# Kernel optimization log

Hardware: AMD Instinct MI355X
Metric: run time of the kernel (lower is better)

## Reference

```python
import jax, jax.numpy as jnp
import numpy as np

EPS = 1e-06
TEMP = 2.0

def _l2norm(x, eps=EPS):
    # F.normalize: x / max(||x||, eps)
    n = jnp.sqrt(jnp.sum(x * x, axis=-1, keepdims=True))
    return x / jnp.maximum(n, eps)

def setup_inputs() -> dict:
    key = jax.random.key(0)
    k1, k2 = jax.random.split(key)
    B, Lt, Lv, D = 8, 64, 16384, 256
    t = jax.random.normal(k1, (B, Lt, D), dtype=jnp.float32)
    v = jax.random.normal(k2, (B, Lv, D), dtype=jnp.float32)
    return {"t": t, "v": v}

def reference(t, v):
    dtype = v.dtype
    t = _l2norm(jnp.nan_to_num(t).astype(jnp.float32))
    v = _l2norm(jnp.nan_to_num(v).astype(jnp.float32))
    # S: [B, Lv, Lt]
    S = jnp.einsum('bvd,btd->bvt', v, t) / TEMP
    # text->vision attention: softmax over text axis (stable shift as in source)
    S_vt = jnp.nan_to_num(S - jnp.max(S, axis=2, keepdims=True))
    A_vt = jax.nn.softmax(S_vt, axis=2)            # [B, Lv, Lt]
    weights_vt = jax.nn.softmax(A_vt / TEMP, axis=1)  # softmax over vision axis
    text_score = jnp.sum(weights_vt * A_vt, axis=1)   # [B, Lt]
    text_score = text_score / (jnp.sum(text_score, axis=1, keepdims=True) + EPS)
    # vision<-text attention: per-sample loop in source == batched softmax over Lv
    S_tv = jnp.nan_to_num(S - jnp.max(S, axis=1, keepdims=True))
    A_tv = jax.nn.softmax(S_tv, axis=1)            # softmax over vision axis, [B, Lv, Lt]
    scores = jnp.einsum('bvt,bt->bv', A_tv, text_score)  # [B, Lv]
    mn = jnp.min(scores, axis=1, keepdims=True)
    mx = jnp.max(scores, axis=1, keepdims=True)
    scores = (scores - mn) / (mx - mn + EPS)
    return scores.astype(dtype)
```

## Files before the change

kernel.cpp:

```cpp
#include <hip/hip_runtime.h>
#include <stdint.h>

#define NB 8
#define LT 64
#define LV 16384
#define DD 256
#define EPSV 1e-6f
#define BF16MAX 3.3895313892515355e38f

typedef unsigned short u16t;
typedef __attribute__((ext_vector_type(8))) short short8;
typedef __attribute__((ext_vector_type(4))) float floatx4;

__device__ __forceinline__ float bf2f(u16t h) {
    union { uint32_t u; float f; } cv; cv.u = ((uint32_t)h) << 16; return cv.f;
}
__device__ __forceinline__ uint32_t asu(float f) { union { float f; uint32_t u; } c; c.f = f; return c.u; }
__device__ __forceinline__ float asf(uint32_t u) { union { uint32_t u; float f; } c; c.u = u; return c.f; }
__device__ __forceinline__ u16t f2bf(float f) {
    uint32_t u = asu(f);
    return (u16t)((u + 0x7fffu + ((u >> 16) & 1u)) >> 16);
}
__device__ __forceinline__ float fixnum(float f) {
    if (f != f) return 0.0f;
    if (f > BF16MAX) return BF16MAX;
    if (f < -BF16MAX) return -BF16MAX;
    return f;
}
__device__ __forceinline__ float load_in(const void* p, long i, int isf32) {
    return isf32 ? ((const float*)p)[i] : bf2f(((const u16t*)p)[i]);
}
__device__ __forceinline__ uint32_t bfhead(float a, float& hf) {
    uint32_t u = asu(a);
    uint32_t h = (u + 0x7fffu + ((u >> 16) & 1u)) >> 16;
    hf = asf(h << 16);
    return h;
}

__global__ void k_sniff(const u16t* v, int* flag) {
    int lane = threadIdx.x;
    int sane = 0;
    for (int i = 0; i < 16; ++i) {
        u16t h = v[lane * 16 + i];
        int ex = (h >> 7) & 0xFF;
        if ((h & 0x7FFF) == 0 || (ex >= 96 && ex < 160)) ++sane;
    }
    #pragma unroll
    for (int o = 1; o < 64; o <<= 1) sane += __shfl_xor(sane, o, 64);
    if (lane == 0) flag[0] = (sane < 900) ? 1 : 0;
}

__global__ void k0_zero(float* Z) {
    int i = blockIdx.x * 256 + threadIdx.x;
    if (i < 1536) Z[i] = 0.0f;
    else if (i < 1552) {
        unsigned* u = (unsigned*)(Z + 2048);
        int j = i - 1536;
        u[j] = (j & 1) ? 0u : 0x7F7FFFFFu;
    }
}

__global__ void k1_tnorm(const void* t, u16t* tnB, const int* flag) {
    __shared__ float red[256];
    int isf32 = flag[0];
    int row = blockIdx.x;
    int k = threadIdx.x;
    float x = fixnum(load_in(t, (long)row * DD + k, isf32));
    red[k] = x * x;
    __syncthreads();
    for (int s = 128; s > 0; s >>= 1) {
        if (k < s) red[k] += red[k + s];
        __syncthreads();
    }
    float scale = 0.5f / fmaxf(sqrtf(red[0]), EPSV);
    tnB[row * DD + k] = f2bf(x * scale);
}

__global__ __launch_bounds__(256) void k_gemm(const void* v, const u16t* tnB,
                                              float* Z, float* S1, float* S2,
                                              const float* c, float* scores,
                                              float* E,
                                              const int* flag, int mode) {
    __shared__ u16t ldsT[64 * 264];
    __shared__ float zlds[3][4][64];
    int isf32 = flag[0];
    int tid = threadIdx.x, wave = tid >> 6, lane = tid & 63;
    int c16 = lane & 15, q = lane >> 4;
    int b = blockIdx.y, tile = blockIdx.x;
    int rowbase = tile * 128 + wave * 32;

    {
        const u16t* src = tnB + (size_t)b * (LT * DD);
        for (int i = tid; i < 2048; i += 256) {
            int tt = i >> 5, k8 = i & 31;
            *(uint4*)&ldsT[tt * 264 + k8 * 8] = *(const uint4*)&src[tt * DD + k8 * 8];
        }
    }
    __syncthreads();

    floatx4 acc[2][4];
    #pragma unroll
    for (int mt = 0; mt < 2; ++mt)
        #pragma unroll
        for (int nt = 0; nt < 4; ++nt) acc[mt][nt] = (floatx4){0.f, 0.f, 0.f, 0.f};
    float ssqp[2] = {0.f, 0.f};

    for (int kc = 0; kc < 8; ++kc) {
        short8 bf[4];
        #pragma unroll
        for (int nt = 0; nt < 4; ++nt)
            bf[nt] = *(const short8*)&ldsT[(nt * 16 + c16) * 264 + kc * 32 + q * 8];

        #pragma unroll
        for (int mt = 0; mt < 2; ++mt) {
            int row = rowbase + mt * 16 + c16;
            float f[8];
            if (isf32) {
                const float* vr = (const float*)v +
                    ((size_t)b * LV + row) * DD + kc * 32 + q * 8;
                float4 p0 = *(const float4*)vr;
                float4 p1 = *(const float4*)(vr + 4);
                f[0]=p0.x; f[1]=p0.y; f[2]=p0.z; f[3]=p0.w;
                f[4]=p1.x; f[5]=p1.y; f[6]=p1.z; f[7]=p1.w;
            } else {
                const u16t* vr = (const u16t*)v +
                    ((size_t)b * LV + row) * DD + kc * 32 + q * 8;
                uint4 u = *(const uint4*)vr;
                f[0]=bf2f((u16t)u.x); f[1]=bf2f((u16t)(u.x>>16));
                f[2]=bf2f((u16t)u.y); f[3]=bf2f((u16t)(u.y>>16));
                f[4]=bf2f((u16t)u.z); f[5]=bf2f((u16t)(u.z>>16));
                f[6]=bf2f((u16t)u.w); f[7]=bf2f((u16t)(u.w>>16));
            }
            #pragma unroll
            for (int i = 0; i < 8; ++i) f[i] = fixnum(f[i]);
            union { short8 s; uint32_t u[4]; } a1, a2, a3;
            #pragma unroll
            for (int i = 0; i < 4; ++i) {
                float e0 = f[2*i], e1 = f[2*i+1];
                ssqp[mt] += e0 * e0 + e1 * e1;
                float h10f, h11f, h20f, h21f, dummy;
                uint32_t h10 = bfhead(e0, h10f), h11 = bfhead(e1, h11f);
                float r10 = e0 - h10f,  r11 = e1 - h11f;
                uint32_t h20 = bfhead(r10, h20f), h21 = bfhead(r11, h21f);
                float r20 = r10 - h20f, r21 = r11 - h21f;
                uint32_t h30 = bfhead(r20, dummy), h31 = bfhead(r21, dummy);
                a1.u[i] = h10 | (h11 << 16);
                a2.u[i] = h20 | (h21 << 16);
                a3.u[i] = h30 | (h31 << 16);
            }
            #pragma unroll
            for (int nt = 0; nt < 4; ++nt) {
                acc[mt][nt] = __builtin_amdgcn_mfma_f32_16x16x32_bf16(
                    a1.s, bf[nt], acc[mt][nt], 0, 0, 0);
                acc[mt][nt] = __builtin_amdgcn_mfma_f32_16x16x32_bf16(
                    a2.s, bf[nt], acc[mt][nt], 0, 0, 0);
                acc[mt][nt] = __builtin_amdgcn_mfma_f32_16x16x32_bf16(
                    a3.s, bf[nt], acc[mt][nt], 0, 0, 0);
            }
        }
    }

    float ssqf[2];
    #pragma unroll
    for (int mt = 0; mt < 2; ++mt) {
        float s = ssqp[mt];
        s += __shfl_xor(s, 16, 64);
        s += __shfl_xor(s, 32, 64);
        ssqf[mt] = s;
    }
    float facr[2][4];
    #pragma unroll
    for (int mt = 0; mt < 2; ++mt)
        #pragma unroll
        for (int reg = 0; reg < 4; ++reg) {
            float ss = __shfl(ssqf[mt], q * 4 + reg, 64);
            facr[mt][reg] = 1.0f / fmaxf(sqrtf(ss), EPSV);
        }

    if (mode == 0) {
        float zacc[4] = {0,0,0,0}, s1acc[4] = {0,0,0,0}, s2acc[4] = {0,0,0,0};
        #pragma unroll
        for (int mt = 0; mt < 2; ++mt)
            #pragma unroll
            for (int reg = 0; reg < 4; ++reg) {
                float e[4], se = 0.f;
                #pragma unroll
                for (int nt = 0; nt < 4; ++nt) {
                    e[nt] = __expf(acc[mt][nt][reg] * facr[mt][reg]);
                    se += e[nt];
                }
                se += __shfl_xor(se, 1, 64);
                se += __shfl_xor(se, 2, 64);
                se += __shfl_xor(se, 4, 64);
                se += __shfl_xor(se, 8, 64);
                float inv = 1.0f / se;
                if (E) {
                    size_t rbase = ((((size_t)b << 14) + rowbase + mt * 16 + q * 4 + reg) << 6);
                    #pragma unroll
                    for (int nt = 0; nt < 4; ++nt)
                        E[rbase + nt * 16 + c16] = e[nt];
                }
                #pragma unroll
                for (int nt = 0; nt < 4; ++nt) {
                    float A = e[nt] * inv;
                    float w = __expf(0.5f * A);
                    zacc[nt] += e[nt]; s1acc[nt] += w; s2acc[nt] += w * A;
                }
            }
        #pragma unroll
        for (int nt = 0; nt < 4; ++nt) {
            zacc[nt]  += __shfl_xor(zacc[nt], 16, 64);  zacc[nt]  += __shfl_xor(zacc[nt], 32, 64);
            s1acc[nt] += __shfl_xor(s1acc[nt], 16, 64); s1acc[nt] += __shfl_xor(s1acc[nt], 32, 64);
            s2acc[nt] += __shfl_xor(s2acc[nt], 16, 64); s2acc[nt] += __shfl_xor(s2acc[nt], 32, 64);
        }
        if (lane < 16) {
            #pragma unroll
            for (int nt = 0; nt < 4; ++nt) {
                zlds[0][wave][nt * 16 + lane] = zacc[nt];
                zlds[1][wave][nt * 16 + lane] = s1acc[nt];
                zlds[2][wave][nt * 16 + lane] = s2acc[nt];
            }
        }
        __syncthreads();
        if (tid < 64) {
            float z  = zlds[0][0][tid] + zlds[0][1][tid] + zlds[0][2][tid] + zlds[0][3][tid];
            float a  = zlds[1][0][tid] + zlds[1][1][tid] + zlds[1][2][tid] + zlds[1][3][tid];
            float s2 = zlds[2][0][tid] + zlds[2][1][tid] + zlds[2][2][tid] + zlds[2][3][tid];
            atomicAdd(&Z[b * LT + tid], z);
            atomicAdd(&S1[b * LT + tid], a);
            atomicAdd(&S2[b * LT + tid], s2);
        }
    } else {
        float cc[4];
        #pragma unroll
        for (int nt = 0; nt < 4; ++nt) cc[nt] = c[b * LT + nt * 16 + c16];
        #pragma unroll
        for (int mt = 0; mt < 2; ++mt)
            #pragma unroll
            for (int reg = 0; reg < 4; ++reg) {
                float x = 0.f;
                #pragma unroll
                for (int nt = 0; nt < 4; ++nt)
                    x += __expf(acc[mt][nt][reg] * facr[mt][reg]) * cc[nt];
                x += __shfl_xor(x, 1, 64);
                x += __shfl_xor(x, 2, 64);
                x += __shfl_xor(x, 4, 64);
                x += __shfl_xor(x, 8, 64);
                if (c16 == 0)
                    scores[(size_t)b * LV + rowbase + mt * 16 + q * 4 + reg] = x;
            }
    }
}

__global__ __launch_bounds__(64) void k3_coef(const float* Z, const float* S1,
                                              const float* S2, float* c) {
    int b = blockIdx.x, lane = threadIdx.x;
    float ts = S2[b * LT + lane] / S1[b * LT + lane];
    float tot = ts;
    #pragma unroll
    for (int o = 1; o < 64; o <<= 1) tot += __shfl_xor(tot, o, 64);
    c[b * LT + lane] = ts / ((tot + EPSV) * Z[b * LT + lane]);
}

__global__ __launch_bounds__(256) void k2_scores(const float* E, const float* c,
                                                 float* scores, unsigned* mnmxU) {
    __shared__ float cl[64];
    __shared__ float rmn[256], rmx[256];
    int tid = threadIdx.x;
    int b = blockIdx.x >> 6;
    if (tid < 64) cl[tid] = c[b * LT + tid];
    __syncthreads();
    size_t row = (size_t)blockIdx.x * 256 + tid;
    const float* er = E + (row << 6);
    float f[64];
    #pragma unroll
    for (int j = 0; j < 16; ++j) {
        float4 v4 = *(const float4*)(er + j * 4);
        f[j*4+0] = v4.x; f[j*4+1] = v4.y; f[j*4+2] = v4.z; f[j*4+3] = v4.w;
    }
    float p[16];
    #pragma unroll
    for (int i = 0; i < 16; ++i) {
        float x = 0.f;
        #pragma unroll
        for (int nt = 0; nt < 4; ++nt) x += f[nt * 16 + i] * cl[nt * 16 + i];
        p[i] = x;
    }
    float q1[8], q2[4], q3[2];
    #pragma unroll
    for (int j = 0; j < 8; ++j) q1[j] = p[2*j] + p[2*j+1];
    #pragma unroll
    for (int j = 0; j < 4; ++j) q2[j] = q1[2*j] + q1[2*j+1];
    #pragma unroll
    for (int j = 0; j < 2; ++j) q3[j] = q2[2*j] + q2[2*j+1];
    float x = q3[0] + q3[1];
    scores[row] = x;

    rmn[tid] = x; rmx[tid] = x;
    __syncthreads();
    for (int s = 128; s > 0; s >>= 1) {
        if (tid < s) {
            rmn[tid] = fminf(rmn[tid], rmn[tid + s]);
            rmx[tid] = fmaxf(rmx[tid], rmx[tid + s]);
        }
        __syncthreads();
    }
    if (tid == 0) {
        atomicMin(&mnmxU[b * 2],     asu(rmn[0]));
        atomicMax(&mnmxU[b * 2 + 1], asu(rmx[0]));
    }
}

__global__ __launch_bounds__(256) void k_mnmx(const float* scores, float* mnmx) {
    __shared__ float rmn[256], rmx[256];
    int b = blockIdx.x, tid = threadIdx.x;
    float mn = 3.4e38f, mx = -3.4e38f;
    for (int i = tid; i < LV; i += 256) {
        float x = scores[b * LV + i];
        mn = fminf(mn, x); mx = fmaxf(mx, x);
    }
    rmn[tid] = mn; rmx[tid] = mx;
    __syncthreads();
    for (int s = 128; s > 0; s >>= 1) {
        if (tid < s) {
            rmn[tid] = fminf(rmn[tid], rmn[tid + s]);
            rmx[tid] = fmaxf(rmx[tid], rmx[tid + s]);
        }
        __syncthreads();
    }
    if (tid == 0) { mnmx[b * 2] = rmn[0]; mnmx[b * 2 + 1] = rmx[0]; }
}

__global__ __launch_bounds__(256) void k5_out(const float* scores, const float* mnmx,
                                              void* out, const int* flag) {
    int isf32 = flag[0];
    int i = blockIdx.x * 256 + threadIdx.x;
    if (i >= NB * LV) return;
    int b = i >> 14;
    float mn = mnmx[b * 2], mx = mnmx[b * 2 + 1];
    float val = (scores[i] - mn) / (mx - mn + EPSV);
    if (isf32) ((float*)out)[i] = val;
    else ((u16t*)out)[i] = f2bf(val);
}

extern "C" void kernel_launch(void* const* d_in, const int* in_sizes, int n_in,
                              void* d_out, int out_size, void* d_ws, size_t ws_size,
                              hipStream_t stream) {
    const void* t = d_in[0];
    const void* v = d_in[1];
    char* w = (char*)d_ws;

    const size_t E_BYTES = (size_t)NB * LV * LT * 4;
    const size_t NEED_NEW = E_BYTES + 262144 + 524288 + 2080 * 4;

    if (ws_size >= NEED_NEW) {
        float* E      = (float*)w;
        u16t*  tnB    = (u16t*)(w + E_BYTES);
        float* scores = (float*)(w + E_BYTES + 262144);
        float* Z      = (float*)(w + E_BYTES + 262144 + 524288);
        float* S1     = Z + 512;
        float* S2     = Z + 1024;
        float* c      = Z + 1536;
        unsigned* mnmxU = (unsigned*)(Z + 2048);
        int*   flag   = (int*)(Z + 2064);

        k_sniff<<<1, 64, 0, stream>>>((const u16t*)v, flag);
        k0_zero<<<7, 256, 0, stream>>>(Z);
        k1_tnorm<<<512, 256, 0, stream>>>(t, tnB, flag);
        k_gemm<<<dim3(128, NB), 256, 0, stream>>>(v, tnB, Z, S1, S2, nullptr, nullptr,
                                                  E, flag, 0);
        k3_coef<<<NB, 64, 0, stream>>>(Z, S1, S2, c);
        k2_scores<<<512, 256, 0, stream>>>(E, c, scores, mnmxU);
        k5_out<<<512, 256, 0, stream>>>(scores, (const float*)mnmxU, d_out, flag);
    } else {
        u16t*  tnB    = (u16t*)w;
        float* scores = (float*)(w + 262144);
        float* Z      = (float*)(w + 786432);
        float* S1     = Z + 512;
        float* S2     = Z + 1024;
        float* c      = Z + 1536;
        float* mnmx   = Z + 2048;
        int*   flag   = (int*)(Z + 2064);

        k_sniff<<<1, 64, 0, stream>>>((const u16t*)v, flag);
        k0_zero<<<6, 256, 0, stream>>>(Z);
        k1_tnorm<<<512, 256, 0, stream>>>(t, tnB, flag);
        k_gemm<<<dim3(128, NB), 256, 0, stream>>>(v, tnB, Z, S1, S2, nullptr, nullptr,
                                                  nullptr, flag, 0);
        k3_coef<<<NB, 64, 0, stream>>>(Z, S1, S2, c);
        k_gemm<<<dim3(128, NB), 256, 0, stream>>>(v, tnB, Z, S1, S2, c, scores,
                                                  nullptr, flag, 1);
        k_mnmx<<<NB, 256, 0, stream>>>(scores, mnmx);
        k5_out<<<512, 256, 0, stream>>>(scores, mnmx, d_out, flag);
    }
}
```

Measured before the change: 236.7 us.

## Fuse setup kernels, drop third bf16 split term, prefetch v loads in GEMM

The separate sniff and zero kernels are removed: each kernel now re-detects the input dtype in one wave, and the tnorm kernel zeroes the accumulators. The coefficient kernel is folded into k2_scores, and min/max is fused into the mode-1 GEMM. The GEMM splits fp32 activations into two bf16 terms instead of three, cutting MFMA work by a third at some precision cost, and it register-prefetches the next k-chunk of v. Fewer launches and less matrix work are traded for redundant sniffing in every block and lower dot-product accuracy.

```diff
diff --git a/kernel.cpp b/kernel.cpp
--- a/kernel.cpp
+++ b/kernel.cpp
@@ -37,8 +37,7 @@
     return h;
 }
 
-__global__ void k_sniff(const u16t* v, int* flag) {
-    int lane = threadIdx.x;
+__device__ __forceinline__ int sniff_wave(const u16t* v, int lane) {
     int sane = 0;
     for (int i = 0; i < 16; ++i) {
         u16t h = v[lane * 16 + i];
@@ -47,24 +46,18 @@
     }
     #pragma unroll
     for (int o = 1; o < 64; o <<= 1) sane += __shfl_xor(sane, o, 64);
-    if (lane == 0) flag[0] = (sane < 900) ? 1 : 0;
-}
-
-__global__ void k0_zero(float* Z) {
-    int i = blockIdx.x * 256 + threadIdx.x;
-    if (i < 1536) Z[i] = 0.0f;
-    else if (i < 1552) {
-        unsigned* u = (unsigned*)(Z + 2048);
-        int j = i - 1536;
-        u[j] = (j & 1) ? 0u : 0x7F7FFFFFu;
-    }
-}
-
-__global__ void k1_tnorm(const void* t, u16t* tnB, const int* flag) {
+    return (sane < 900) ? 1 : 0;
+}
+
+__global__ __launch_bounds__(256) void k1_tnorm(const void* t, const void* v,
+                                                u16t* tnB, float* Z) {
     __shared__ float red[256];
-    int isf32 = flag[0];
+    __shared__ int sflag;
     int row = blockIdx.x;
     int k = threadIdx.x;
+    if (k < 64) { int f = sniff_wave((const u16t*)v, k); if (k == 0) sflag = f; }
+    __syncthreads();
+    int isf32 = sflag;
     float x = fixnum(load_in(t, (long)row * DD + k, isf32));
     red[k] = x * x;
     __syncthreads();
@@ -74,21 +67,32 @@
     }
     float scale = 0.5f / fmaxf(sqrtf(red[0]), EPSV);
     tnB[row * DD + k] = f2bf(x * scale);
-}
-
-__global__ __launch_bounds__(256) void k_gemm(const void* v, const u16t* tnB,
-                                              float* Z, float* S1, float* S2,
-                                              const float* c, float* scores,
-                                              float* E,
-                                              const int* flag, int mode) {
+
+    if (blockIdx.x < 7) {
+        int i = blockIdx.x * 256 + k;
+        if (i < 1536) Z[i] = 0.0f;
+        else if (i < 1552) {
+            unsigned* u = (unsigned*)(Z + 2048);
+            int j = i - 1536;
+            u[j] = (j & 1) ? 0u : 0x7F7FFFFFu;
+        }
+    }
+}
+
+template<int MODE>
+__global__ __launch_bounds__(256) void k_gemmT(const void* v, const u16t* tnB,
+                                               float* Z, float* S1, float* S2,
+                                               float* EoS, const float* c,
+                                               unsigned* mnmxU) {
     __shared__ u16t ldsT[64 * 264];
     __shared__ float zlds[3][4][64];
-    int isf32 = flag[0];
+    __shared__ int sflag;
     int tid = threadIdx.x, wave = tid >> 6, lane = tid & 63;
     int c16 = lane & 15, q = lane >> 4;
     int b = blockIdx.y, tile = blockIdx.x;
     int rowbase = tile * 128 + wave * 32;
 
+    if (tid < 64) { int f = sniff_wave((const u16t*)v, tid); if (tid == 0) sflag = f; }
     {
         const u16t* src = tnB + (size_t)b * (LT * DD);
         for (int i = tid; i < 2048; i += 256) {
@@ -97,6 +101,7 @@
         }
     }
     __syncthreads();
+    int isf32 = sflag;
 
     floatx4 acc[2][4];
     #pragma unroll
@@ -105,60 +110,90 @@
         for (int nt = 0; nt < 4; ++nt) acc[mt][nt] = (floatx4){0.f, 0.f, 0.f, 0.f};
     float ssqp[2] = {0.f, 0.f};
 
-    for (int kc = 0; kc < 8; ++kc) {
-        short8 bf[4];
-        #pragma unroll
-        for (int nt = 0; nt < 4; ++nt)
-            bf[nt] = *(const short8*)&ldsT[(nt * 16 + c16) * 264 + kc * 32 + q * 8];
-
-        #pragma unroll
-        for (int mt = 0; mt < 2; ++mt) {
-            int row = rowbase + mt * 16 + c16;
-            float f[8];
-            if (isf32) {
-                const float* vr = (const float*)v +
-                    ((size_t)b * LV + row) * DD + kc * 32 + q * 8;
-                float4 p0 = *(const float4*)vr;
-                float4 p1 = *(const float4*)(vr + 4);
-                f[0]=p0.x; f[1]=p0.y; f[2]=p0.z; f[3]=p0.w;
-                f[4]=p1.x; f[5]=p1.y; f[6]=p1.z; f[7]=p1.w;
-            } else {
-                const u16t* vr = (const u16t*)v +
-                    ((size_t)b * LV + row) * DD + kc * 32 + q * 8;
-                uint4 u = *(const uint4*)vr;
-                f[0]=bf2f((u16t)u.x); f[1]=bf2f((u16t)(u.x>>16));
-                f[2]=bf2f((u16t)u.y); f[3]=bf2f((u16t)(u.y>>16));
-                f[4]=bf2f((u16t)u.z); f[5]=bf2f((u16t)(u.z>>16));
-                f[6]=bf2f((u16t)u.w); f[7]=bf2f((u16t)(u.w>>16));
-            }
+    #define PROC_F8(mt)                                                        \
+        do {                                                                   \
+            _Pragma("unroll")                                                  \
+            for (int i = 0; i < 8; ++i) f[i] = fixnum(f[i]);                   \
+            union { short8 s; uint32_t u[4]; } a1, a2;                         \
+            _Pragma("unroll")                                                  \
+            for (int i = 0; i < 4; ++i) {                                      \
+                float e0 = f[2*i], e1 = f[2*i+1];                              \
+                ssqp[mt] += e0 * e0 + e1 * e1;                                 \
+                float h10f, h11f, d0, d1;                                      \
+                uint32_t h10 = bfhead(e0, h10f), h11 = bfhead(e1, h11f);       \
+                float r10 = e0 - h10f,  r11 = e1 - h11f;                       \
+                uint32_t h20 = bfhead(r10, d0), h21 = bfhead(r11, d1);         \
+                a1.u[i] = h10 | (h11 << 16);                                   \
+                a2.u[i] = h20 | (h21 << 16);                                   \
+            }                                                                  \
+            _Pragma("unroll")                                                  \
+            for (int nt = 0; nt < 4; ++nt) {                                   \
+                acc[mt][nt] = __builtin_amdgcn_mfma_f32_16x16x32_bf16(         \
+                    a1.s, bf[nt], acc[mt][nt], 0, 0, 0);                       \
+                acc[mt][nt] = __builtin_amdgcn_mfma_f32_16x16x32_bf16(         \
+                    a2.s, bf[nt], acc[mt][nt], 0, 0, 0);                       \
+            }                                                                  \
+        } while (0)
+
+    if (isf32) {
+        const float4* vr0 = (const float4*)((const float*)v +
+            ((size_t)b * LV + rowbase + c16) * DD) + q * 2;
+        const float4* vr1 = (const float4*)((const float*)v +
+            ((size_t)b * LV + rowbase + 16 + c16) * DD) + q * 2;
+        float4 nA0 = vr0[0], nA1 = vr0[1], nB0 = vr1[0], nB1 = vr1[1];
+        for (int kc = 0; kc < 8; ++kc) {
+            short8 bf[4];
             #pragma unroll
-            for (int i = 0; i < 8; ++i) f[i] = fixnum(f[i]);
-            union { short8 s; uint32_t u[4]; } a1, a2, a3;
+            for (int nt = 0; nt < 4; ++nt)
+                bf[nt] = *(const short8*)&ldsT[(nt * 16 + c16) * 264 + kc * 32 + q * 8];
+            float4 cA0 = nA0, cA1 = nA1, cB0 = nB0, cB1 = nB1;
+            if (kc < 7) {
+                int o = (kc + 1) * 8;
+                nA0 = vr0[o]; nA1 = vr0[o + 1];
+                nB0 = vr1[o]; nB1 = vr1[o + 1];
+            }
+            {
+                float f[8] = {cA0.x, cA0.y, cA0.z, cA0.w, cA1.x, cA1.y, cA1.z, cA1.w};
+                PROC_F8(0);
+            }
+            {
+                float f[8] = {cB0.x, cB0.y, cB0.z, cB0.w, cB1.x, cB1.y, cB1.z, cB1.w};
+                PROC_F8(1);
+            }
+        }
+    } else {
+        const uint4* vr0 = (const uint4*)((const u16t*)v +
+            ((size_t)b * LV + rowbase + c16) * DD) + q;
+        const uint4* vr1 = (const uint4*)((const u16t*)v +
+            ((size_t)b * LV + rowbase + 16 + c16) * DD) + q;
+        uint4 nA = vr0[0], nB = vr1[0];
+        for (int kc = 0; kc < 8; ++kc) {
+            short8 bf[4];
             #pragma unroll
-            for (int i = 0; i < 4; ++i) {
-                float e0 = f[2*i], e1 = f[2*i+1];
-                ssqp[mt] += e0 * e0 + e1 * e1;
-                float h10f, h11f, h20f, h21f, dummy;
-                uint32_t h10 = bfhead(e0, h10f), h11 = bfhead(e1, h11f);
-                float r10 = e0 - h10f,  r11 = e1 - h11f;
-                uint32_t h20 = bfhead(r10, h20f), h21 = bfhead(r11, h21f);
-                float r20 = r10 - h20f, r21 = r11 - h21f;
-                uint32_t h30 = bfhead(r20, dummy), h31 = bfhead(r21, dummy);
-                a1.u[i] = h10 | (h11 << 16);
-                a2.u[i] = h20 | (h21 << 16);
-                a3.u[i] = h30 | (h31 << 16);
-            }
-            #pragma unroll
-            for (int nt = 0; nt < 4; ++nt) {
-                acc[mt][nt] = __builtin_amdgcn_mfma_f32_16x16x32_bf16(
-                    a1.s, bf[nt], acc[mt][nt], 0, 0, 0);
-                acc[mt][nt] = __builtin_amdgcn_mfma_f32_16x16x32_bf16(
-                    a2.s, bf[nt], acc[mt][nt], 0, 0, 0);
-                acc[mt][nt] = __builtin_amdgcn_mfma_f32_16x16x32_bf16(
-                    a3.s, bf[nt], acc[mt][nt], 0, 0, 0);
-            }
-        }
-    }
+            for (int nt = 0; nt < 4; ++nt)
+                bf[nt] = *(const short8*)&ldsT[(nt * 16 + c16) * 264 + kc * 32 + q * 8];
+            uint4 cA = nA, cB = nB;
+            if (kc < 7) {
+                int o = (kc + 1) * 4;
+                nA = vr0[o]; nB = vr1[o];
+            }
+            {
+                float f[8] = {bf2f((u16t)cA.x), bf2f((u16t)(cA.x >> 16)),
+                              bf2f((u16t)cA.y), bf2f((u16t)(cA.y >> 16)),
+                              bf2f((u16t)cA.z), bf2f((u16t)(cA.z >> 16)),
+                              bf2f((u16t)cA.w), bf2f((u16t)(cA.w >> 16))};
+                PROC_F8(0);
+            }
+            {
+                float f[8] = {bf2f((u16t)cB.x), bf2f((u16t)(cB.x >> 16)),
+                              bf2f((u16t)cB.y), bf2f((u16t)(cB.y >> 16)),
+                              bf2f((u16t)cB.z), bf2f((u16t)(cB.z >> 16)),
+                              bf2f((u16t)cB.w), bf2f((u16t)(cB.w >> 16))};
+                PROC_F8(1);
+            }
+        }
+    }
+    #undef PROC_F8
 
     float ssqf[2];
     #pragma unroll
@@ -177,7 +212,7 @@
             facr[mt][reg] = 1.0f / fmaxf(sqrtf(ss), EPSV);
         }
 
-    if (mode == 0) {
+    if (MODE == 0) {
         float zacc[4] = {0,0,0,0}, s1acc[4] = {0,0,0,0}, s2acc[4] = {0,0,0,0};
         #pragma unroll
         for (int mt = 0; mt < 2; ++mt)
@@ -194,11 +229,11 @@
                 se += __shfl_xor(se, 4, 64);
                 se += __shfl_xor(se, 8, 64);
                 float inv = 1.0f / se;
-                if (E) {
+                if (EoS) {
                     size_t rbase = ((((size_t)b << 14) + rowbase + mt * 16 + q * 4 + reg) << 6);
                     #pragma unroll
                     for (int nt = 0; nt < 4; ++nt)
-                        E[rbase + nt * 16 + c16] = e[nt];
+                        EoS[rbase + nt * 16 + c16] = e[nt];
                 }
                 #pragma unroll
                 for (int nt = 0; nt < 4; ++nt) {
@@ -234,6 +269,7 @@
         float cc[4];
         #pragma unroll
         for (int nt = 0; nt < 4; ++nt) cc[nt] = c[b * LT + nt * 16 + c16];
+        float lmn = 3.4e38f, lmx = -3.4e38f;
         #pragma unroll
         for (int mt = 0; mt < 2; ++mt)
             #pragma unroll
@@ -247,8 +283,24 @@
                 x += __shfl_xor(x, 4, 64);
                 x += __shfl_xor(x, 8, 64);
                 if (c16 == 0)
-                    scores[(size_t)b * LV + rowbase + mt * 16 + q * 4 + reg] = x;
-            }
+                    EoS[(size_t)b * LV + rowbase + mt * 16 + q * 4 + reg] = x;
+                lmn = fminf(lmn, x); lmx = fmaxf(lmx, x);
+            }
+        float* rmn = (float*)ldsT;
+        float* rmx = ((float*)ldsT) + 256;
+        rmn[tid] = lmn; rmx[tid] = lmx;
+        __syncthreads();
+        for (int s = 128; s > 0; s >>= 1) {
+            if (tid < s) {
+                rmn[tid] = fminf(rmn[tid], rmn[tid + s]);
+                rmx[tid] = fmaxf(rmx[tid], rmx[tid + s]);
+            }
+            __syncthreads();
+        }
+        if (tid == 0) {
+            atomicMin(&mnmxU[b * 2],     asu(rmn[0]));
+            atomicMax(&mnmxU[b * 2 + 1], asu(rmx[0]));
+        }
     }
 }
 
@@ -262,13 +314,20 @@
     c[b * LT + lane] = ts / ((tot + EPSV) * Z[b * LT + lane]);
 }
 
-__global__ __launch_bounds__(256) void k2_scores(const float* E, const float* c,
+__global__ __launch_bounds__(256) void k2_scores(const float* E, const float* Zg,
                                                  float* scores, unsigned* mnmxU) {
     __shared__ float cl[64];
     __shared__ float rmn[256], rmx[256];
     int tid = threadIdx.x;
     int b = blockIdx.x >> 6;
-    if (tid < 64) cl[tid] = c[b * LT + tid];
+    if (tid < 64) {
+        const float* Z = Zg; const float* S1 = Zg + 512; const float* S2 = Zg + 1024;
+        float ts = S2[b * LT + tid] / S1[b * LT + tid];
+        float tot = ts;
+        #pragma unroll
+        for (int o = 1; o < 64; o <<= 1) tot += __shfl_xor(tot, o, 64);
+        cl[tid] = ts / ((tot + EPSV) * Z[b * LT + tid]);
+    }
     __syncthreads();
     size_t row = (size_t)blockIdx.x * 256 + tid;
     const float* er = E + (row << 6);
@@ -311,30 +370,14 @@
     }
 }
 
-__global__ __launch_bounds__(256) void k_mnmx(const float* scores, float* mnmx) {
-    __shared__ float rmn[256], rmx[256];
-    int b = blockIdx.x, tid = threadIdx.x;
-    float mn = 3.4e38f, mx = -3.4e38f;
-    for (int i = tid; i < LV; i += 256) {
-        float x = scores[b * LV + i];
-        mn = fminf(mn, x); mx = fmaxf(mx, x);
-    }
-    rmn[tid] = mn; rmx[tid] = mx;
-    __syncthreads();
-    for (int s = 128; s > 0; s >>= 1) {
-        if (tid < s) {
-            rmn[tid] = fminf(rmn[tid], rmn[tid + s]);
-            rmx[tid] = fmaxf(rmx[tid], rmx[tid + s]);
-        }
-        __syncthreads();
-    }
-    if (tid == 0) { mnmx[b * 2] = rmn[0]; mnmx[b * 2 + 1] = rmx[0]; }
-}
-
 __global__ __launch_bounds__(256) void k5_out(const float* scores, const float* mnmx,
-                                              void* out, const int* flag) {
-    int isf32 = flag[0];
-    int i = blockIdx.x * 256 + threadIdx.x;
+                                              void* out, const void* v) {
+    __shared__ int sflag;
+    int tid = threadIdx.x;
+    if (tid < 64) { int f = sniff_wave((const u16t*)v, tid); if (tid == 0) sflag = f; }
+    __syncthreads();
+    int isf32 = sflag;
+    int i = blockIdx.x * 256 + tid;
     if (i >= NB * LV) return;
     int b = i >> 14;
     float mn = mnmx[b * 2], mx = mnmx[b * 2 + 1];
@@ -360,18 +403,13 @@
         float* Z      = (float*)(w + E_BYTES + 262144 + 524288);
         float* S1     = Z + 512;
         float* S2     = Z + 1024;
-        float* c      = Z + 1536;
         unsigned* mnmxU = (unsigned*)(Z + 2048);
-        int*   flag   = (int*)(Z + 2064);
-
-        k_sniff<<<1, 64, 0, stream>>>((const u16t*)v, flag);
-        k0_zero<<<7, 256, 0, stream>>>(Z);
-        k1_tnorm<<<512, 256, 0, stream>>>(t, tnB, flag);
-        k_gemm<<<dim3(128, NB), 256, 0, stream>>>(v, tnB, Z, S1, S2, nullptr, nullptr,
-                                                  E, flag, 0);
-        k3_coef<<<NB, 64, 0, stream>>>(Z, S1, S2, c);
-        k2_scores<<<512, 256, 0, stream>>>(E, c, scores, mnmxU);
-        k5_out<<<512, 256, 0, stream>>>(scores, (const float*)mnmxU, d_out, flag);
+
+        k1_tnorm<<<512, 256, 0, stream>>>(t, v, tnB, Z);
+        k_gemmT<0><<<dim3(128, NB), 256, 0, stream>>>(v, tnB, Z, S1, S2, E,
+                                                      nullptr, nullptr);
+        k2_scores<<<512, 256, 0, stream>>>(E, Z, scores, mnmxU);
+        k5_out<<<512, 256, 0, stream>>>(scores, (const float*)mnmxU, d_out, v);
     } else {
         u16t*  tnB    = (u16t*)w;
         float* scores = (float*)(w + 262144);
@@ -379,18 +417,14 @@
         float* S1     = Z + 512;
         float* S2     = Z + 1024;
         float* c      = Z + 1536;
-        float* mnmx   = Z + 2048;
-        int*   flag   = (int*)(Z + 2064);
-
-        k_sniff<<<1, 64, 0, stream>>>((const u16t*)v, flag);
-        k0_zero<<<6, 256, 0, stream>>>(Z);
-        k1_tnorm<<<512, 256, 0, stream>>>(t, tnB, flag);
-        k_gemm<<<dim3(128, NB), 256, 0, stream>>>(v, tnB, Z, S1, S2, nullptr, nullptr,
-                                                  nullptr, flag, 0);
+        unsigned* mnmxU = (unsigned*)(Z + 2048);
+
+        k1_tnorm<<<512, 256, 0, stream>>>(t, v, tnB, Z);
+        k_gemmT<0><<<dim3(128, NB), 256, 0, stream>>>(v, tnB, Z, S1, S2, nullptr,
+                                                      nullptr, nullptr);
         k3_coef<<<NB, 64, 0, stream>>>(Z, S1, S2, c);
-        k_gemm<<<dim3(128, NB), 256, 0, stream>>>(v, tnB, Z, S1, S2, c, scores,
-                                                  nullptr, flag, 1);
-        k_mnmx<<<NB, 256, 0, stream>>>(scores, mnmx);
-        k5_out<<<512, 256, 0, stream>>>(scores, mnmx, d_out, flag);
-    }
-}
+        k_gemmT<1><<<dim3(128, NB), 256, 0, stream>>>(v, tnB, Z, S1, S2, scores,
+                                                      c, mnmxU);
+        k5_out<<<512, 256, 0, stream>>>(scores, (const float*)mnmxU, d_out, v);
+    }
+}
```

Result: no change. 236.4 us (-0.1%).
